# Kernel tuning notes

Hardware: AMD Instinct MI355X
Metric: run time of the kernel (lower is better)

## Reference

```python
import jax, jax.numpy as jnp
import numpy as np

NEG_SLOPE = 0.2  # PyG GATConv default negative_slope
EPS = 1e-16     # PyG softmax denominator epsilon


def gat_conv(x, src, dst, W, a_src, a_dst, bias):
    """PyG GATConv (concat=True, dropout off). x:[N,Fin], src/dst:[E]."""
    N = x.shape[0]
    H, C = a_src.shape
    h = (x @ W).reshape(N, H, C)                      # per-head projected features
    es = jnp.einsum('nhc,hc->nh', h, a_src)           # alpha_src per node/head
    ed = jnp.einsum('nhc,hc->nh', h, a_dst)           # alpha_dst per node/head
    e = jax.nn.leaky_relu(es[src] + ed[dst], NEG_SLOPE)   # [E,H] edge scores
    # segment softmax over destination nodes (every node has a self loop)
    m = jax.ops.segment_max(e, dst, num_segments=N)
    p = jnp.exp(e - m[dst])
    denom = jax.ops.segment_sum(p, dst, num_segments=N)
    alpha = p / (denom[dst] + EPS)                    # [E,H]
    out = jax.ops.segment_sum(h[src] * alpha[:, :, None], dst, num_segments=N)
    return out.reshape(N, H * C) + bias


def _single_graph(x, ei, W1, a_src1, a_dst1, b1, W2, a_src2, a_dst2, b2):
    N = x.shape[0]
    loop = jnp.arange(N, dtype=ei.dtype)              # add_self_loops=True
    src = jnp.concatenate([ei[0], loop])
    dst = jnp.concatenate([ei[1], loop])
    h = jax.nn.relu(gat_conv(x, src, dst, W1, a_src1, a_dst1, b1))
    # F.dropout with p=0.0 is identity
    return gat_conv(h, src, dst, W2, a_src2, a_dst2, b2)


def setup_inputs() -> dict:
    key = jax.random.key(0)
    ks = jax.random.split(key, 9)
    B, N, E, F_in, H, C = 2, 20000, 320000, 128, 8, 64

    def glorot(k, shape):
        fan_in, fan_out = shape[-2] if len(shape) > 1 else shape[-1], shape[-1]
        s = np.sqrt(6.0 / (fan_in + fan_out)).astype(np.float32)
        return jax.random.uniform(k, shape, jnp.float32, -s, s)

    return {
        'xs': jax.random.normal(ks[0], (B, N, F_in), jnp.float32),
        'edge_indexs': jax.random.randint(ks[1], (B, 2, E), 0, N, jnp.int32),
        'W1': glorot(ks[2], (F_in, H * C)),
        'a_src1': glorot(ks[3], (H, C)),
        'a_dst1': glorot(ks[4], (H, C)),
        'b1': jnp.zeros((H * C,), jnp.float32),
        'W2': glorot(ks[5], (H * C, C)),
        'a_src2': glorot(ks[6], (1, C)),
        'a_dst2': glorot(ks[7], (1, C)),
        'b2': jnp.zeros((C,), jnp.float32),
    }


def reference(xs, edge_indexs, W1, a_src1, a_dst1, b1, W2, a_src2, a_dst2, b2):
    f = lambda x, ei: _single_graph(x, ei, W1, a_src1, a_dst1, b1, W2, a_src2, a_dst2, b2)
    return jax.vmap(f)(xs, edge_indexs)               # [B, N, C]
```

## Files before the change

### kernel.cpp

```cpp
#include <hip/hip_runtime.h>
#include <hip/hip_bf16.h>
#include <cstdint>

#define NEG_SLOPE 0.2f
#define SOFTMAX_EPS 1e-16f
#define NN 20000
#define EE 320000
#define CAP 48

typedef __hip_bfloat16 bf16;
typedef unsigned short ushort;
typedef short s8v __attribute__((ext_vector_type(8)));
typedef float f4v __attribute__((ext_vector_type(4)));
typedef float f2v __attribute__((ext_vector_type(2)));

static __device__ __forceinline__ float lo16(unsigned u) { return __uint_as_float(u << 16); }
static __device__ __forceinline__ float hi16(unsigned u) { return __uint_as_float(u & 0xffff0000u); }
static __device__ __forceinline__ ushort f2bf(float v) {
    bf16 h = __float2bfloat16(v);
    return *(ushort*)&h;
}

__global__ void prep_kernel(const float* __restrict__ W1, const float* __restrict__ W2,
                            ushort* __restrict__ w1hi, ushort* __restrict__ w1lo,
                            ushort* __restrict__ w2hi, ushort* __restrict__ w2lo,
                            int* __restrict__ count) {
    int bid = blockIdx.x;
    int t = threadIdx.x;
    if (bid >= 48) {
        int idx = (bid - 48) * 256 + t;
        if (idx < 2 * NN) count[idx] = 0;
        return;
    }
    __shared__ float T[32][65];
    const float* src; ushort *dhi, *dlo; int K, C, c0, k0;
    if (bid < 32) { src = W1; dhi = w1hi; dlo = w1lo; K = 128; C = 512; c0 = (bid & 7) * 64; k0 = (bid >> 3) * 32; }
    else          { src = W2; dhi = w2hi; dlo = w2lo; K = 512; C = 64;  c0 = 0;              k0 = (bid - 32) * 32; }
    for (int i = 0; i < 8; ++i) {
        int flat = t + i * 256;
        int k = flat >> 6, c = flat & 63;
        T[k][c] = src[(size_t)(k0 + k) * C + c0 + c];
    }
    __syncthreads();
    int c = t >> 2, j0 = (t & 3) * 8;
    unsigned hp[4], lp[4];
#pragma unroll
    for (int p = 0; p < 4; ++p) {
        float v0 = T[j0 + p * 2][c], v1 = T[j0 + p * 2 + 1][c];
        ushort h0 = f2bf(v0), h1 = f2bf(v1);
        float l0 = v0 - __uint_as_float((unsigned)h0 << 16);
        float l1 = v1 - __uint_as_float((unsigned)h1 << 16);
        hp[p] = (unsigned)h0 | ((unsigned)h1 << 16);
        lp[p] = (unsigned)f2bf(l0) | ((unsigned)f2bf(l1) << 16);
    }
    size_t o = (size_t)(c0 + c) * K + k0 + j0;
    *(uint4*)&dhi[o] = make_uint4(hp[0], hp[1], hp[2], hp[3]);
    *(uint4*)&dlo[o] = make_uint4(lp[0], lp[1], lp[2], lp[3]);
}

#define G1S 40
#define GEMM1_BLOCKS 1252
__global__ __launch_bounds__(256) void gemm1_scatter(
        const float* __restrict__ xs, const ushort* __restrict__ w1hi,
        const ushort* __restrict__ w1lo, const float* __restrict__ a_src,
        const float* __restrict__ a_dst, bf16* __restrict__ h1,
        float* __restrict__ es, float* __restrict__ ed,
        const int* __restrict__ ei, int* __restrict__ count,
        ushort* __restrict__ esrc) {
    __shared__ ushort lds[25600];
    int t = threadIdx.x;
    int bid = blockIdx.x;

    if (bid >= GEMM1_BLOCKS) {
        int idx = bid - GEMM1_BLOCKS;
        int b = idx / 1250;
        int e = (idx % 1250) * 256 + t;
        const int* srcA = ei + (size_t)b * 2 * EE;
        int s = srcA[e], d = srcA[EE + e];
        if ((unsigned)d >= NN || (unsigned)s >= NN) return;
        int pos = atomicAdd(&count[b * NN + d], 1);
        if (pos < CAP)
            esrc[((size_t)b * NN + d) * CAP + pos] = (ushort)s;
        return;
    }

    ushort* Xhi = lds;
    ushort* Xlo = lds + 2560;
    ushort* Whi = lds + 5120;
    ushort* Wlo = lds + 15360;
    int w = t >> 6, lane = t & 63, quad = lane >> 4, l16 = lane & 15;
    int b = bid / 626;
    int rem = bid % 626;
    int nhalf = rem / 313;
    int row0 = (rem % 313) * 64, nbase = nhalf * 256;
    const float* x = xs + (size_t)b * NN * 128;
    bf16*  h1b = h1 + (size_t)b * NN * 512;
    float* esb = es + (size_t)b * NN * 8;
    float* edb = ed + (size_t)b * NN * 8;

    f4v acc[16];
#pragma unroll
    for (int i = 0; i < 16; ++i) acc[i] = (f4v)0.f;

    for (int kc = 0; kc < 4; ++kc) {
        __syncthreads();
        {
            int row = t >> 2, c0 = (t & 3) * 8;
            float v[8];
            if (row0 + row < NN) {
                float4 A = *(const float4*)&x[(size_t)(row0 + row) * 128 + kc * 32 + c0];
                float4 B = *(const float4*)&x[(size_t)(row0 + row) * 128 + kc * 32 + c0 + 4];
                v[0] = A.x; v[1] = A.y; v[2] = A.z; v[3] = A.w;
                v[4] = B.x; v[5] = B.y; v[6] = B.z; v[7] = B.w;
            } else {
#pragma unroll
                for (int i = 0; i < 8; ++i) v[i] = 0.f;
            }
            unsigned hp[4], lp[4];
#pragma unroll
            for (int p = 0; p < 4; ++p) {
                ushort h0 = f2bf(v[p * 2]), h1_ = f2bf(v[p * 2 + 1]);
                float l0 = v[p * 2] - __uint_as_float((unsigned)h0 << 16);
                float l1 = v[p * 2 + 1] - __uint_as_float((unsigned)h1_ << 16);
                hp[p] = (unsigned)h0 | ((unsigned)h1_ << 16);
                lp[p] = (unsigned)f2bf(l0) | ((unsigned)f2bf(l1) << 16);
            }
            *(uint4*)&Xhi[row * G1S + c0] = make_uint4(hp[0], hp[1], hp[2], hp[3]);
            *(uint4*)&Xlo[row * G1S + c0] = make_uint4(lp[0], lp[1], lp[2], lp[3]);
        }
        {
            const ushort* sh = w1hi + (size_t)(nbase + t) * 128 + kc * 32;
            const ushort* sl = w1lo + (size_t)(nbase + t) * 128 + kc * 32;
            uint4 h0 = *(const uint4*)(sh), h1_ = *(const uint4*)(sh + 8);
            uint4 h2 = *(const uint4*)(sh + 16), h3 = *(const uint4*)(sh + 24);
            uint4 l0 = *(const uint4*)(sl), l1 = *(const uint4*)(sl + 8);
            uint4 l2 = *(const uint4*)(sl + 16), l3 = *(const uint4*)(sl + 24);
            *(uint4*)&Whi[t * G1S]      = h0; *(uint4*)&Whi[t * G1S + 8]  = h1_;
            *(uint4*)&Whi[t * G1S + 16] = h2; *(uint4*)&Whi[t * G1S + 24] = h3;
            *(uint4*)&Wlo[t * G1S]      = l0; *(uint4*)&Wlo[t * G1S + 8]  = l1;
            *(uint4*)&Wlo[t * G1S + 16] = l2; *(uint4*)&Wlo[t * G1S + 24] = l3;
        }
        __syncthreads();
        int arow = (w * 16 + l16) * G1S + quad * 8;
        s8v ahi = *(const s8v*)&Xhi[arow];
        s8v alo = *(const s8v*)&Xlo[arow];
#pragma unroll
        for (int ct = 0; ct < 16; ++ct) {
            int baddr = (ct * 16 + l16) * G1S + quad * 8;
            s8v bhi = *(const s8v*)&Whi[baddr];
            s8v blo = *(const s8v*)&Wlo[baddr];
            acc[ct] = __builtin_amdgcn_mfma_f32_16x16x32_bf16(ahi, bhi, acc[ct], 0, 0, 0);
            acc[ct] = __builtin_amdgcn_mfma_f32_16x16x32_bf16(ahi, blo, acc[ct], 0, 0, 0);
            acc[ct] = __builtin_amdgcn_mfma_f32_16x16x32_bf16(alo, bhi, acc[ct], 0, 0, 0);
        }
    }

#pragma unroll
    for (int hh = 0; hh < 4; ++hh) {
        float s4[4] = {0.f, 0.f, 0.f, 0.f}, d4[4] = {0.f, 0.f, 0.f, 0.f};
#pragma unroll
        for (int ct4 = 0; ct4 < 4; ++ct4) {
            int ct = hh * 4 + ct4;
            int c = nbase + ct * 16 + l16;
            float as = a_src[c], ad = a_dst[c];
#pragma unroll
            for (int r = 0; r < 4; ++r) { s4[r] += acc[ct][r] * as; d4[r] += acc[ct][r] * ad; }
        }
#pragma unroll
        for (int o = 1; o < 16; o <<= 1) {
#pragma unroll
            for (int r = 0; r < 4; ++r) {
                s4[r] += __shfl_xor(s4[r], o);
                d4[r] += __shfl_xor(d4[r], o);
            }
        }
        if (l16 == 0) {
            int head = nhalf * 4 + hh;
#pragma unroll
            for (int r = 0; r < 4; ++r) {
                int gr = row0 + w * 16 + quad * 4 + r;
                if (gr < NN) { esb[gr * 8 + head] = s4[r]; edb[gr * 8 + head] = d4[r]; }
            }
        }
    }

    __syncthreads();
    ushort* rp = lds + w * 4224;
#pragma unroll
    for (int ct = 0; ct < 16; ++ct)
#pragma unroll
        for (int r = 0; r < 4; ++r)
            rp[(quad * 4 + r) * 264 + ct * 16 + l16] = f2bf(acc[ct][r]);
#pragma unroll
    for (int i = 0; i < 8; ++i) {
        int idx = i * 512 + lane * 8;
        int row = idx >> 8, col = idx & 255;
        uint4 vv = *(const uint4*)&rp[row * 264 + col];
        int gr = row0 + w * 16 + row;
        if (gr < NN) *(uint4*)&h1b[(size_t)gr * 512 + nbase + col] = vv;
    }
}

#define G2S 72
__global__ __launch_bounds__(256) void gemm2_mfma(
        const bf16* __restrict__ a, const ushort* __restrict__ w2hi,
        const ushort* __restrict__ w2lo, const float* __restrict__ a_src,
        const float* __restrict__ a_dst, bf16* __restrict__ h2,
        float* __restrict__ es, float* __restrict__ ed) {
    __shared__ ushort lds[13824];
    ushort* AS  = lds;
    ushort* Whi = lds + 4608;
    ushort* Wlo = lds + 9216;

    int t = threadIdx.x;
    int w = t >> 6, lane = t & 63, quad = lane >> 4, l16 = lane & 15;
    int b = blockIdx.y;
    int row0 = blockIdx.x * 64;
    const bf16* ab = a + (size_t)b * NN * 512;
    bf16*  h2b = h2 + (size_t)b * NN * 64;
    float* esb = es + (size_t)b * NN;
    float* edb = ed + (size_t)b * NN;

    f4v acc[4];
#pragma unroll
    for (int i = 0; i < 4; ++i) acc[i] = (f4v)0.f;

    for (int kc = 0; kc < 8; ++kc) {
        __syncthreads();
        {
            int row = t >> 2, k0 = (t & 3) * 16;
            uint4 q0, q1;
            if (row0 + row < NN) {
                q0 = *(const uint4*)(ab + (size_t)(row0 + row) * 512 + kc * 64 + k0);
                q1 = *(const uint4*)(ab + (size_t)(row0 + row) * 512 + kc * 64 + k0 + 8);
            } else { q0 = make_uint4(0, 0, 0, 0); q1 = q0; }
            *(uint4*)&AS[row * G2S + k0]     = q0;
            *(uint4*)&AS[row * G2S + k0 + 8] = q1;
            const ushort* sh = w2hi + (size_t)row * 512 + kc * 64 + k0;
            const ushort* sl = w2lo + (size_t)row * 512 + kc * 64 + k0;
            *(uint4*)&Whi[row * G2S + k0]     = *(const uint4*)(sh);
            *(uint4*)&Whi[row * G2S + k0 + 8] = *(const uint4*)(sh + 8);
            *(uint4*)&Wlo[row * G2S + k0]     = *(const uint4*)(sl);
            *(uint4*)&Wlo[row * G2S + k0 + 8] = *(const uint4*)(sl + 8);
        }
        __syncthreads();
#pragma unroll
        for (int ks = 0; ks < 2; ++ks) {
            s8v av = *(const s8v*)&AS[(w * 16 + l16) * G2S + ks * 32 + quad * 8];
#pragma unroll
            for (int ct = 0; ct < 4; ++ct) {
                int baddr = (ct * 16 + l16) * G2S + ks * 32 + quad * 8;
                s8v bhi = *(const s8v*)&Whi[baddr];
                s8v blo = *(const s8v*)&Wlo[baddr];
                acc[ct] = __builtin_amdgcn_mfma_f32_16x16x32_bf16(av, bhi, acc[ct], 0, 0, 0);
                acc[ct] = __builtin_amdgcn_mfma_f32_16x16x32_bf16(av, blo, acc[ct], 0, 0, 0);
            }
        }
    }

    {
        float s4[4] = {0.f, 0.f, 0.f, 0.f}, d4[4] = {0.f, 0.f, 0.f, 0.f};
#pragma unroll
        for (int ct = 0; ct < 4; ++ct) {
            int c = ct * 16 + l16;
            float as = a_src[c], ad = a_dst[c];
#pragma unroll
            for (int r = 0; r < 4; ++r) { s4[r] += acc[ct][r] * as; d4[r] += acc[ct][r] * ad; }
        }
#pragma unroll
        for (int o = 1; o < 16; o <<= 1) {
#pragma unroll
            for (int r = 0; r < 4; ++r) {
                s4[r] += __shfl_xor(s4[r], o);
                d4[r] += __shfl_xor(d4[r], o);
            }
        }
        if (l16 == 0) {
#pragma unroll
            for (int r = 0; r < 4; ++r) {
                int gr = row0 + w * 16 + quad * 4 + r;
                if (gr < NN) { esb[gr] = s4[r]; edb[gr] = d4[r]; }
            }
        }
    }

    __syncthreads();
    ushort* rp = lds + w * 1152;
#pragma unroll
    for (int ct = 0; ct < 4; ++ct)
#pragma unroll
        for (int r = 0; r < 4; ++r)
            rp[(quad * 4 + r) * G2S + ct * 16 + l16] = f2bf(acc[ct][r]);
#pragma unroll
    for (int i = 0; i < 2; ++i) {
        int idx = i * 512 + lane * 8;
        int row = idx >> 6, col = idx & 63;
        uint4 vv = *(const uint4*)&rp[row * G2S + col];
        int gr = row0 + w * 16 + row;
        if (gr < NN) *(uint4*)&h2b[(size_t)gr * 64 + col] = vv;
    }
}

__global__ __launch_bounds__(256) void aggregate1_kernel(
        const bf16* __restrict__ h1, const float* __restrict__ es,
        const float* __restrict__ ed, const int* __restrict__ count,
        const ushort* __restrict__ esrc, const float* __restrict__ b1,
        bf16* __restrict__ out1) {
    __shared__ float alds[4][2][60];
    __shared__ unsigned offs[4][60];

    int t = threadIdx.x;
    int wv = t >> 6, lane = t & 63;
    int bid = blockIdx.x;
    int combo = bid & 7;
    int b = combo >> 2;
    int qtr = combo & 3;
    int q = bid >> 3;
    int n = q * 4 + wv;

    const bf16*  h1b = h1 + (size_t)b * NN * 512;
    const float* esb = es + (size_t)b * NN * 8;
    const float* edb = ed + (size_t)b * NN * 8;
    bf16* out1b = out1 + (size_t)b * NN * 512;

    int deg_e = count[b * NN + n];
    deg_e = max(0, min(deg_e, CAP));
    int deg = deg_e + 1;
    size_t beg = ((size_t)b * NN + n) * CAP;

    float2 edv = *(const float2*)&edb[n * 8 + qtr * 2];
    float edh[2] = {edv.x, edv.y};

    bool act = lane < deg;
    int sreg = act ? ((lane < deg_e) ? (int)esrc[beg + lane] : n) : 0;
    const char* eb = (const char*)esb;
    unsigned eoff = ((unsigned)sreg << 5) + (unsigned)qtr * 8u;
    float2 s0 = *(const float2*)(eb + eoff);
    float e[2] = {s0.x, s0.y};
    float m[2], p[2], sum[2];
#pragma unroll
    for (int h = 0; h < 2; ++h) {
        float v = e[h] + edh[h];
        v = (v >= 0.f) ? v : NEG_SLOPE * v;
        e[h] = act ? v : -1e30f;
        m[h] = e[h];
    }
#pragma unroll
    for (int o = 32; o > 0; o >>= 1) {
#pragma unroll
        for (int h = 0; h < 2; ++h) m[h] = fmaxf(m[h], __shfl_xor(m[h], o));
    }
#pragma unroll
    for (int h = 0; h < 2; ++h) { p[h] = act ? __expf(e[h] - m[h]) : 0.f; sum[h] = p[h]; }
#pragma unroll
    for (int o = 32; o > 0; o >>= 1) {
#pragma unroll
        for (int h = 0; h < 2; ++h) sum[h] += __shfl_xor(sum[h], o);
    }
    if (lane < 60) {
        offs[wv][lane] = act ? ((unsigned)sreg << 10) : 0u;
#pragma unroll
        for (int h = 0; h < 2; ++h)
            alds[wv][h][lane] = p[h] / (sum[h] + SOFTMAX_EPS);
    }

    int mh = lane >> 5;
    unsigned l4b = (unsigned)qtr * 256u + (unsigned)lane * 4u;
    const bf16* hb = h1b;
    int trips = (deg + 3) >> 2;
    int trips2 = (trips + 1) & ~1;

    f2v acc0 = {0.f, 0.f};
    unsigned A0, A1, A2, A3, B0, B1, B2, B3;
    float4 wA, wB;

#define GLOAD(dst, voff) \
    asm volatile("global_load_dword %0, %1, %2" : "=&v"(dst) : "v"(voff), "s"(hb))

#define LOADBANK(U0, U1, U2, U3, W4, blk) do { \
        int s_ = (blk) << 2; \
        uint4 ov_ = *(const uint4*)&offs[wv][s_]; \
        W4 = *(const float4*)&alds[wv][mh][s_]; \
        unsigned va_ = ov_.x + l4b, vb_ = ov_.y + l4b; \
        unsigned vc_ = ov_.z + l4b, vd_ = ov_.w + l4b; \
        GLOAD(U0, va_); GLOAD(U1, vb_); GLOAD(U2, vc_); GLOAD(U3, vd_); \
    } while (0)

#define WAITSB(nlit) do { \
        asm volatile("s_waitcnt vmcnt(" #nlit ")" ::: "memory"); \
        __builtin_amdgcn_sched_barrier(0); \
    } while (0)

#define ROW(U, W) do { \
        f2v wp_ = {W, W}; \
        f2v t0_ = {lo16(U), hi16(U)}; acc0 += t0_ * wp_; \
    } while (0)

#define CONSUME(U0, U1, U2, U3, W4) do { \
        ROW(U0, W4.x); ROW(U1, W4.y); ROW(U2, W4.z); ROW(U3, W4.w); \
    } while (0)

    LOADBANK(A0, A1, A2, A3, wA, 0);
    LOADBANK(B0, B1, B2, B3, wB, 1);
    for (int it = 0; it + 2 < trips2; it += 2) {
        WAITSB(4);
        CONSUME(A0, A1, A2, A3, wA); LOADBANK(A0, A1, A2, A3, wA, it + 2);
        WAITSB(4);
        CONSUME(B0, B1, B2, B3, wB); LOADBANK(B0, B1, B2, B3, wB, it + 3);
    }
    WAITSB(4);
    CONSUME(A0, A1, A2, A3, wA);
    WAITSB(0);
    CONSUME(B0, B1, B2, B3, wB);

#undef GLOAD
#undef LOADBANK
#undef WAITSB
#undef ROW
#undef CONSUME

    float2 bv = *(const float2*)&b1[qtr * 128 + lane * 2];
    union { ushort us[2]; unsigned u1; } pack;
    pack.us[0] = f2bf(fmaxf(acc0.x + bv.x, 0.f));
    pack.us[1] = f2bf(fmaxf(acc0.y + bv.y, 0.f));
    *(unsigned*)(out1b + (size_t)n * 512 + qtr * 128 + lane * 2) = pack.u1;
}

__global__ void aggregate2_kernel(const bf16* __restrict__ h2, const float* __restrict__ es,
                                  const float* __restrict__ ed, const int* __restrict__ count,
                                  const ushort* __restrict__ esrc, const float* __restrict__ bias2,
                                  float* __restrict__ out) {
    __shared__ float wl[4][64];
    __shared__ int slidx[4][64];
    int t = threadIdx.x;
    int wv = t >> 6, lane = t & 63;
    int bid = blockIdx.x;
    int xcd = bid & 7;
    int q = bid >> 3;
    int b = xcd >> 2;
    int n = (xcd & 3) * 5000 + q * 4 + wv;

    const bf16*  h2b = h2 + (size_t)b * NN * 64;
    const float* esb = es + (size_t)b * NN;
    const float* edb = ed + (size_t)b * NN;
    float* outb = out + (size_t)b * NN * 64;

    int deg_e = count[b * NN + n];
    deg_e = max(0, min(deg_e, CAP));
    int deg = deg_e + 1;
    size_t beg = ((size_t)b * NN + n) * CAP;
    float edn = edb[n];

    bool act = lane < deg;
    int sreg = act ? ((lane < deg_e) ? (int)esrc[beg + lane] : n) : 0;
    float ev = act ? esb[sreg] + edn : -1e30f;
    ev = (ev >= 0.f) ? ev : NEG_SLOPE * ev;
    if (!act) ev = -1e30f;
    float m = ev;
#pragma unroll
    for (int o = 32; o > 0; o >>= 1) m = fmaxf(m, __shfl_xor(m, o));
    float p = act ? __expf(ev - m) : 0.f;
    float sum = p;
#pragma unroll
    for (int o = 32; o > 0; o >>= 1) sum += __shfl_xor(sum, o);
    slidx[wv][lane] = sreg;
    wl[wv][lane] = p / (sum + SOFTMAX_EPS);

    float acc[4] = {0.f, 0.f, 0.f, 0.f};
    int grp = lane >> 4, ch4 = (lane & 15) * 4;
    int j = grp;
    for (; j + 4 < deg; j += 8) {
        int sA = slidx[wv][j];     float wA = wl[wv][j];
        int sB = slidx[wv][j + 4]; float wB = wl[wv][j + 4];
        uint2 uA = *(const uint2*)(h2b + (size_t)sA * 64 + ch4);
        uint2 uB = *(const uint2*)(h2b + (size_t)sB * 64 + ch4);
        acc[0] += wA * lo16(uA.x); acc[1] += wA * hi16(uA.x);
        acc[2] += wA * lo16(uA.y); acc[3] += wA * hi16(uA.y);
        acc[0] += wB * lo16(uB.x); acc[1] += wB * hi16(uB.x);
        acc[2] += wB * lo16(uB.y); acc[3] += wB * hi16(uB.y);
    }
    for (; j < deg; j += 4) {
        int s = slidx[wv][j];
        float wt = wl[wv][j];
        uint2 u = *(const uint2*)(h2b + (size_t)s * 64 + ch4);
        acc[0] += wt * lo16(u.x); acc[1] += wt * hi16(u.x);
        acc[2] += wt * lo16(u.y); acc[3] += wt * hi16(u.y);
    }
#pragma unroll
    for (int i = 0; i < 4; ++i) {
        acc[i] += __shfl_xor(acc[i], 16);
        acc[i] += __shfl_xor(acc[i], 32);
    }
    if (lane < 16) {
        float4 o4;
        o4.x = acc[0] + bias2[ch4 + 0];
        o4.y = acc[1] + bias2[ch4 + 1];
        o4.z = acc[2] + bias2[ch4 + 2];
        o4.w = acc[3] + bias2[ch4 + 3];
        *(float4*)&outb[(size_t)n * 64 + ch4] = o4;
    }
}

extern "C" void kernel_launch(void* const* d_in, const int* in_sizes, int n_in,
                              void* d_out, int out_size, void* d_ws, size_t ws_size,
                              hipStream_t stream) {
    const float* xs     = (const float*)d_in[0];
    const int*   ei     = (const int*)d_in[1];
    const float* W1     = (const float*)d_in[2];
    const float* a_src1 = (const float*)d_in[3];
    const float* a_dst1 = (const float*)d_in[4];
    const float* b1     = (const float*)d_in[5];
    const float* W2     = (const float*)d_in[6];
    const float* a_src2 = (const float*)d_in[7];
    const float* a_dst2 = (const float*)d_in[8];
    const float* b2     = (const float*)d_in[9];
    float* out = (float*)d_out;

    const int B = 2;

    uintptr_t p = (uintptr_t)d_ws;
    auto alloc = [&](size_t bytes) {
        void* r = (void*)p;
        p += (bytes + 255) & ~(size_t)255;
        return r;
    };
    bf16* h1   = (bf16*)alloc((size_t)B * NN * 512 * 2);
    bf16* out1 = (bf16*)alloc((size_t)B * NN * 512 * 2);
    char* unionA = (char*)alloc((size_t)B * NN * 64 * 2);
    float*  es1   = (float*)unionA;
    float*  ed1   = (float*)(unionA + 1280000);
    ushort* wt1hi = (ushort*)(unionA + 2560000);
    ushort* wt1lo = (ushort*)(unionA + 2560000 + 131072);
    bf16*   h2    = (bf16*)unionA;
    ushort* wt2hi = (ushort*)alloc((size_t)64 * 512 * 2);
    ushort* wt2lo = (ushort*)alloc((size_t)64 * 512 * 2);
    float* es2    = (float*)alloc((size_t)B * NN * 4);
    float* ed2    = (float*)alloc((size_t)B * NN * 4);
    int*   count  = (int*)alloc((size_t)B * NN * 4);
    ushort* esrc  = (ushort*)alloc((size_t)B * NN * CAP * 2);

    const int initBlocks = (2 * NN + 255) / 256;
    prep_kernel<<<48 + initBlocks, 256, 0, stream>>>(W1, W2, wt1hi, wt1lo, wt2hi, wt2lo, count);
    gemm1_scatter<<<GEMM1_BLOCKS + 2500, 256, 0, stream>>>(xs, wt1hi, wt1lo, a_src1, a_dst1,
                                                           h1, es1, ed1, ei, count, esrc);
    aggregate1_kernel<<<40000, 256, 0, stream>>>(h1, es1, ed1, count, esrc, b1, out1);
    gemm2_mfma<<<dim3(313, B), 256, 0, stream>>>(out1, wt2hi, wt2lo, a_src2, a_dst2, h2, es2, ed2);
    aggregate2_kernel<<<10000, 256, 0, stream>>>(h2, es2, ed2, count, esrc, b2, out);
}
```

Measured before the change: 258.6 us.

## Process two destination nodes per wave in layer-1 aggregation with dwordx2 gathers

Each wavefront in aggregate1 now handles two destination nodes, one per half-wave of 32 lanes. The softmax reductions run over 16-lane xor shuffles, and each lane gathers 4 bf16 features with dwordx2 loads, so the grid is halved. The aim is to cut per-node wave overhead (softmax setup, launch) and issue wider memory transactions. Nodes with more than 31 edges take a slower serial fallback path, and the paired nodes share a loop trip count set by the larger degree.

```diff
diff --git a/kernel.cpp b/kernel.cpp
--- a/kernel.cpp
+++ b/kernel.cpp
@@ -306,8 +306,8 @@
         const float* __restrict__ ed, const int* __restrict__ count,
         const ushort* __restrict__ esrc, const float* __restrict__ b1,
         bf16* __restrict__ out1) {
-    __shared__ float alds[4][2][60];
-    __shared__ unsigned offs[4][60];
+    __shared__ float alds[4][2][2][32];
+    __shared__ unsigned offs[4][2][32];
 
     int t = threadIdx.x;
     int wv = t >> 6, lane = t & 63;
@@ -315,74 +315,118 @@
     int combo = bid & 7;
     int b = combo >> 2;
     int qtr = combo & 3;
-    int q = bid >> 3;
-    int n = q * 4 + wv;
+    int nA = (bid >> 3) * 8 + wv * 2;
+    int nd = lane >> 5;
+    int slot = lane & 31;
+    int n_lane = nA + nd;
 
     const bf16*  h1b = h1 + (size_t)b * NN * 512;
     const float* esb = es + (size_t)b * NN * 8;
     const float* edb = ed + (size_t)b * NN * 8;
     bf16* out1b = out1 + (size_t)b * NN * 512;
 
-    int deg_e = count[b * NN + n];
-    deg_e = max(0, min(deg_e, CAP));
-    int deg = deg_e + 1;
-    size_t beg = ((size_t)b * NN + n) * CAP;
-
-    float2 edv = *(const float2*)&edb[n * 8 + qtr * 2];
-    float edh[2] = {edv.x, edv.y};
-
-    bool act = lane < deg;
-    int sreg = act ? ((lane < deg_e) ? (int)esrc[beg + lane] : n) : 0;
-    const char* eb = (const char*)esb;
-    unsigned eoff = ((unsigned)sreg << 5) + (unsigned)qtr * 8u;
-    float2 s0 = *(const float2*)(eb + eoff);
-    float e[2] = {s0.x, s0.y};
-    float m[2], p[2], sum[2];
-#pragma unroll
-    for (int h = 0; h < 2; ++h) {
-        float v = e[h] + edh[h];
-        v = (v >= 0.f) ? v : NEG_SLOPE * v;
-        e[h] = act ? v : -1e30f;
-        m[h] = e[h];
-    }
-#pragma unroll
-    for (int o = 32; o > 0; o >>= 1) {
-#pragma unroll
-        for (int h = 0; h < 2; ++h) m[h] = fmaxf(m[h], __shfl_xor(m[h], o));
-    }
-#pragma unroll
-    for (int h = 0; h < 2; ++h) { p[h] = act ? __expf(e[h] - m[h]) : 0.f; sum[h] = p[h]; }
-#pragma unroll
-    for (int o = 32; o > 0; o >>= 1) {
-#pragma unroll
-        for (int h = 0; h < 2; ++h) sum[h] += __shfl_xor(sum[h], o);
-    }
-    if (lane < 60) {
-        offs[wv][lane] = act ? ((unsigned)sreg << 10) : 0u;
-#pragma unroll
-        for (int h = 0; h < 2; ++h)
-            alds[wv][h][lane] = p[h] / (sum[h] + SOFTMAX_EPS);
-    }
-
-    int mh = lane >> 5;
-    unsigned l4b = (unsigned)qtr * 256u + (unsigned)lane * 4u;
+    int deg_e_lane = count[b * NN + n_lane];
+    deg_e_lane = max(0, min(deg_e_lane, CAP));
+    int degAe = __shfl(deg_e_lane, 0);
+    int degBe = __shfl(deg_e_lane, 32);
+
+    if (degAe > 31 || degBe > 31) {
+        unsigned cb64 = (unsigned)qtr * 256u + (unsigned)lane * 4u;
+        for (int k = 0; k < 2; ++k) {
+            int nn = nA + k;
+            int de = count[b * NN + nn];
+            de = max(0, min(de, CAP));
+            int dg = de + 1;
+            bool act2 = lane < dg;
+            int sr = act2 ? ((lane < de) ? (int)esrc[((size_t)b * NN + nn) * CAP + lane] : nn) : 0;
+            float2 edv2 = *(const float2*)&edb[nn * 8 + qtr * 2];
+            float2 esv2 = *(const float2*)((const char*)esb + ((unsigned)sr << 5) + (unsigned)qtr * 8u);
+            float e0 = esv2.x + edv2.x; e0 = (e0 >= 0.f) ? e0 : NEG_SLOPE * e0; e0 = act2 ? e0 : -1e30f;
+            float e1 = esv2.y + edv2.y; e1 = (e1 >= 0.f) ? e1 : NEG_SLOPE * e1; e1 = act2 ? e1 : -1e30f;
+            float m0 = e0, m1 = e1;
+#pragma unroll
+            for (int o = 32; o > 0; o >>= 1) {
+                m0 = fmaxf(m0, __shfl_xor(m0, o));
+                m1 = fmaxf(m1, __shfl_xor(m1, o));
+            }
+            float p0 = act2 ? __expf(e0 - m0) : 0.f;
+            float p1 = act2 ? __expf(e1 - m1) : 0.f;
+            float s0 = p0, s1 = p1;
+#pragma unroll
+            for (int o = 32; o > 0; o >>= 1) {
+                s0 += __shfl_xor(s0, o);
+                s1 += __shfl_xor(s1, o);
+            }
+            float a0 = p0 / (s0 + SOFTMAX_EPS);
+            float a1 = p1 / (s1 + SOFTMAX_EPS);
+            f2v acc = {0.f, 0.f};
+            for (int j = 0; j < dg; ++j) {
+                int sj = __shfl(sr, j);
+                float aw0 = __shfl(a0, j);
+                float aw1 = __shfl(a1, j);
+                float aw = (lane >= 32) ? aw1 : aw0;
+                unsigned u = *(const unsigned*)((const char*)h1b + ((unsigned)sj << 10) + cb64);
+                f2v tv = {lo16(u), hi16(u)};
+                f2v wp2 = {aw, aw};
+                acc += tv * wp2;
+            }
+            float2 bv2 = *(const float2*)&b1[qtr * 128 + lane * 2];
+            union { ushort us[2]; unsigned u1; } pk;
+            pk.us[0] = f2bf(fmaxf(acc.x + bv2.x, 0.f));
+            pk.us[1] = f2bf(fmaxf(acc.y + bv2.y, 0.f));
+            *(unsigned*)(out1b + (size_t)nn * 512 + qtr * 128 + lane * 2) = pk.u1;
+        }
+        return;
+    }
+
+    int deg = deg_e_lane + 1;
+    bool act = slot < deg;
+    size_t beg = ((size_t)b * NN + n_lane) * CAP;
+    int sreg = act ? ((slot < deg_e_lane) ? (int)esrc[beg + slot] : n_lane) : 0;
+    float2 edv = *(const float2*)&edb[n_lane * 8 + qtr * 2];
+    float2 esv = *(const float2*)((const char*)esb + ((unsigned)sreg << 5) + (unsigned)qtr * 8u);
+    float e0 = esv.x + edv.x; e0 = (e0 >= 0.f) ? e0 : NEG_SLOPE * e0; e0 = act ? e0 : -1e30f;
+    float e1 = esv.y + edv.y; e1 = (e1 >= 0.f) ? e1 : NEG_SLOPE * e1; e1 = act ? e1 : -1e30f;
+    float m0 = e0, m1 = e1;
+#pragma unroll
+    for (int o = 16; o > 0; o >>= 1) {
+        m0 = fmaxf(m0, __shfl_xor(m0, o));
+        m1 = fmaxf(m1, __shfl_xor(m1, o));
+    }
+    float p0 = act ? __expf(e0 - m0) : 0.f;
+    float p1 = act ? __expf(e1 - m1) : 0.f;
+    float s0 = p0, s1 = p1;
+#pragma unroll
+    for (int o = 16; o > 0; o >>= 1) {
+        s0 += __shfl_xor(s0, o);
+        s1 += __shfl_xor(s1, o);
+    }
+    offs[wv][nd][slot] = act ? ((unsigned)sreg << 10) : 0u;
+    alds[wv][nd][0][slot] = p0 / (s0 + SOFTMAX_EPS);
+    alds[wv][nd][1][slot] = p1 / (s1 + SOFTMAX_EPS);
+
+    int mh = slot >> 4;
+    const unsigned* op = &offs[wv][nd][0];
+    const float*    wp = &alds[wv][nd][mh][0];
+    unsigned cb = (unsigned)qtr * 256u + (unsigned)slot * 8u;
     const bf16* hb = h1b;
-    int trips = (deg + 3) >> 2;
+    int mdeg = max(degAe, degBe) + 1;
+    int trips = (mdeg + 3) >> 2;
     int trips2 = (trips + 1) & ~1;
 
-    f2v acc0 = {0.f, 0.f};
-    unsigned A0, A1, A2, A3, B0, B1, B2, B3;
+    f2v acc0 = {0.f, 0.f}, acc1 = {0.f, 0.f};
+    uint2 A0, A1, A2, A3, B0, B1, B2, B3;
     float4 wA, wB;
 
 #define GLOAD(dst, voff) \
-    asm volatile("global_load_dword %0, %1, %2" : "=&v"(dst) : "v"(voff), "s"(hb))
+    asm volatile("global_load_dwordx2 %0, %1, %2" : "=&v"(dst) : "v"(voff), "s"(hb))
 
 #define LOADBANK(U0, U1, U2, U3, W4, blk) do { \
         int s_ = (blk) << 2; \
-        uint4 ov_ = *(const uint4*)&offs[wv][s_]; \
-        W4 = *(const float4*)&alds[wv][mh][s_]; \
-        unsigned va_ = ov_.x + l4b, vb_ = ov_.y + l4b; \
-        unsigned vc_ = ov_.z + l4b, vd_ = ov_.w + l4b; \
+        uint4 ov_ = *(const uint4*)&op[s_]; \
+        W4 = *(const float4*)&wp[s_]; \
+        unsigned va_ = ov_.x + cb, vb_ = ov_.y + cb; \
+        unsigned vc_ = ov_.z + cb, vd_ = ov_.w + cb; \
         GLOAD(U0, va_); GLOAD(U1, vb_); GLOAD(U2, vc_); GLOAD(U3, vd_); \
     } while (0)
 
@@ -393,7 +437,8 @@
 
 #define ROW(U, W) do { \
         f2v wp_ = {W, W}; \
-        f2v t0_ = {lo16(U), hi16(U)}; acc0 += t0_ * wp_; \
+        f2v t0_ = {lo16(U.x), hi16(U.x)}; acc0 += t0_ * wp_; \
+        f2v t1_ = {lo16(U.y), hi16(U.y)}; acc1 += t1_ * wp_; \
     } while (0)
 
 #define CONSUME(U0, U1, U2, U3, W4) do { \
@@ -419,11 +464,13 @@
 #undef ROW
 #undef CONSUME
 
-    float2 bv = *(const float2*)&b1[qtr * 128 + lane * 2];
-    union { ushort us[2]; unsigned u1; } pack;
+    float4 bv = *(const float4*)&b1[qtr * 128 + slot * 4];
+    union { ushort us[4]; uint2 u2; } pack;
     pack.us[0] = f2bf(fmaxf(acc0.x + bv.x, 0.f));
     pack.us[1] = f2bf(fmaxf(acc0.y + bv.y, 0.f));
-    *(unsigned*)(out1b + (size_t)n * 512 + qtr * 128 + lane * 2) = pack.u1;
+    pack.us[2] = f2bf(fmaxf(acc1.x + bv.z, 0.f));
+    pack.us[3] = f2bf(fmaxf(acc1.y + bv.w, 0.f));
+    *(uint2*)(out1b + (size_t)n_lane * 512 + qtr * 128 + slot * 4) = pack.u2;
 }
 
 __global__ void aggregate2_kernel(const bf16* __restrict__ h2, const float* __restrict__ es,
@@ -543,7 +590,7 @@
     prep_kernel<<<48 + initBlocks, 256, 0, stream>>>(W1, W2, wt1hi, wt1lo, wt2hi, wt2lo, count);
     gemm1_scatter<<<GEMM1_BLOCKS + 2500, 256, 0, stream>>>(xs, wt1hi, wt1lo, a_src1, a_dst1,
                                                            h1, es1, ed1, ei, count, esrc);
-    aggregate1_kernel<<<40000, 256, 0, stream>>>(h1, es1, ed1, count, esrc, b1, out1);
+    aggregate1_kernel<<<20000, 256, 0, stream>>>(h1, es1, ed1, count, esrc, b1, out1);
     gemm2_mfma<<<dim3(313, B), 256, 0, stream>>>(out1, wt2hi, wt2lo, a_src2, a_dst2, h2, es2, ed2);
     aggregate2_kernel<<<10000, 256, 0, stream>>>(h2, es2, ed2, count, esrc, b2, out);
 }
```

Result: no change. 258.2 us (-0.1%).
